# Kernel optimization log

Hardware: AMD Instinct MI355X
Metric: run time of the kernel (lower is better)

## Reference

```python
import jax, jax.numpy as jnp
import numpy as np

B, LE, LD = 8, 4096, 4096
DE, DD, A = 512, 512, 128


def setup_inputs() -> dict:
    key = jax.random.key(0)
    ks = jax.random.split(key, 9)
    f32 = jnp.float32
    return {
        "encoder_outputs": jax.random.normal(ks[0], (B, LE, DE), f32),
        "decoder_outputs": jax.random.normal(ks[1], (B, LD, DD), f32),
        # linear_q / linear_k / linear_v (Dense with bias, relu activation)
        "Wq": jax.random.normal(ks[2], (DD, A), f32) * 0.05,
        "bq": jnp.zeros((A,), f32),
        "Wk": jax.random.normal(ks[3], (DE, A), f32) * 0.05,
        "bk": jnp.zeros((A,), f32),
        "Wv": jax.random.normal(ks[4], (DE, A), f32) * 0.05,
        "bv": jnp.zeros((A,), f32),
        # perceptron branch weights (Dense, no bias)
        "Pw": jax.random.normal(ks[5], (A, A), f32) * 0.05,
        "Pu": jax.random.normal(ks[6], (A, A), f32) * 0.05,
        "pv": jax.random.normal(ks[7], (A, 1), f32) * 0.05,
    }


def reference(encoder_outputs, decoder_outputs, Wq, bq, Wk, bk, Wv, bv, Pw, Pu, pv):
    att = Wq.shape[1]
    q = jax.nn.relu(decoder_outputs @ Wq + bq)   # [B, Ld, A]
    k = jax.nn.relu(encoder_outputs @ Wk + bk)   # [B, Le, A]
    v = jax.nn.relu(encoder_outputs @ Wv + bv)   # [B, Le, A]
    # perceptron score: pv^T (Pw q_i + Pu k_j). No nonlinearity between the
    # sum and pv, so it decomposes additively -> no [B,Ld,Le,A] tiling needed.
    q_term = (q @ Pw) @ pv                        # [B, Ld, 1]
    k_term = (k @ Pu) @ pv                        # [B, Le, 1]
    scores = (q_term + jnp.swapaxes(k_term, 1, 2)) / jnp.sqrt(jnp.float32(att))  # [B, Ld, Le]
    weights = jax.nn.softmax(scores, axis=-1)
    attention = jnp.einsum('bij,bjd->bid', weights, v)  # [B, Ld, A]
    return attention
```

## Files before the change

kernel.cpp:

```cpp
#include <hip/hip_runtime.h>
#include <hip/hip_bf16.h>

#define B_   8
#define LE_  4096
#define LD_  4096
#define KDIM 512
#define AA_  128
#define RTOT (B_*LE_)
#define NDIM 256

typedef __attribute__((ext_vector_type(8))) short short8;
typedef __attribute__((ext_vector_type(4))) float f32x4;

#define WCT_OFF   0
#define U_OFF     262144
#define BIAS_OFF  262656
#define NUM_OFF   263680
#define S_OFF     267776
#define WN_OFF    398848
#define VB_OFF    529920

__device__ inline ushort f2bf(float f) {
    union { float f; unsigned u; } x; x.f = f;
    unsigned r = x.u + 0x7fffu + ((x.u >> 16) & 1u);
    return (ushort)(r >> 16);
}
__device__ inline float bf2f(ushort s) {
    union { unsigned u; float f; } x; x.u = ((unsigned)s) << 16;
    return x.f;
}

__global__ void prep_kernel(const float* __restrict__ Wk, const float* __restrict__ bk,
                            const float* __restrict__ Wv, const float* __restrict__ bv,
                            const float* __restrict__ Pu, const float* __restrict__ pv,
                            ushort* __restrict__ wct, float* __restrict__ u,
                            float* __restrict__ bias, float* __restrict__ num) {
    int t = threadIdx.x;
    int base = blockIdx.x * 256 + t;
    for (int i = 0; i < 4; ++i) {
        int idx = base + i * 32768;
        int n = idx >> 9, k = idx & 511;
        float s = (n < 128) ? Wk[k * 128 + n] : Wv[k * 128 + (n - 128)];
        wct[idx] = f2bf(s);
    }
    if (blockIdx.x == 0) {
        if (t < 128) {
            float acc = 0.f;
            for (int c = 0; c < 128; ++c) acc += Pu[t * 128 + c] * pv[c];
            u[t] = acc;
        }
        bias[t] = (t < 128) ? bk[t] : bv[t - 128];
        for (int i = 0; i < 4; ++i) num[t + i * 256] = 0.f;
    }
}

__global__ __launch_bounds__(512, 4)
void gemm_fused(const float* __restrict__ enc, const ushort* __restrict__ wct,
                const float* __restrict__ bias, const float* __restrict__ u,
                ushort* __restrict__ vbuf, float* __restrict__ sout) {
    __shared__ ushort As[64][72];
    __shared__ ushort Bs[256][72];
    __shared__ float s_red[64][2];
    const int t = threadIdx.x;
    const int wv = t >> 6, l = t & 63;
    const int wm = wv >> 2, wn = wv & 3;
    const int m = l & 15, kb = l >> 4;
    const int row0 = blockIdx.x * 64;

    f32x4 acc[2][4] = {};

    for (int k0 = 0; k0 < KDIM; k0 += 64) {
        {
            int r = t >> 3, k8 = (t & 7) * 8;
            const float4* src = (const float4*)(enc + (size_t)(row0 + r) * KDIM + k0 + k8);
            float4 a0 = src[0], a1 = src[1];
            int4 pk;
            pk.x = (int)f2bf(a0.x) | ((int)f2bf(a0.y) << 16);
            pk.y = (int)f2bf(a0.z) | ((int)f2bf(a0.w) << 16);
            pk.z = (int)f2bf(a1.x) | ((int)f2bf(a1.y) << 16);
            pk.w = (int)f2bf(a1.z) | ((int)f2bf(a1.w) << 16);
            *(int4*)&As[r][k8] = pk;
        }
#pragma unroll
        for (int i = 0; i < 4; ++i) {
            int c = t + i * 512;
            int n = c >> 3, k8 = (c & 7) * 8;
            *(int4*)&Bs[n][k8] = *(const int4*)(wct + (size_t)n * KDIM + k0 + k8);
        }
        __syncthreads();
#pragma unroll
        for (int kc = 0; kc < 2; ++kc) {
            short8 afr[2], bfr[4];
#pragma unroll
            for (int mt = 0; mt < 2; ++mt)
                afr[mt] = *(const short8*)&As[wm * 32 + mt * 16 + m][kc * 32 + kb * 8];
#pragma unroll
            for (int nt = 0; nt < 4; ++nt)
                bfr[nt] = *(const short8*)&Bs[wn * 64 + nt * 16 + m][kc * 32 + kb * 8];
#pragma unroll
            for (int mt = 0; mt < 2; ++mt)
#pragma unroll
                for (int nt = 0; nt < 4; ++nt)
                    acc[mt][nt] = __builtin_amdgcn_mfma_f32_16x16x32_bf16(
                        afr[mt], bfr[nt], acc[mt][nt], 0, 0, 0);
        }
        __syncthreads();
    }

    const int rg = l >> 4;
    if (wn >= 2) {
#pragma unroll
        for (int mt = 0; mt < 2; ++mt) {
#pragma unroll
            for (int nt = 0; nt < 4; ++nt) {
                int col = wn * 64 + nt * 16 + m;
                float bsv = bias[col];
#pragma unroll
                for (int j = 0; j < 4; ++j) {
                    int rowl = wm * 32 + mt * 16 + rg * 4 + j;
                    float v = acc[mt][nt][j] + bsv;
                    v = v > 0.f ? v : 0.f;
                    vbuf[(size_t)(row0 + rowl) * AA_ + (col - 128)] = f2bf(v);
                }
            }
        }
    } else {
#pragma unroll
        for (int mt = 0; mt < 2; ++mt) {
            float p[4] = {0.f, 0.f, 0.f, 0.f};
#pragma unroll
            for (int nt = 0; nt < 4; ++nt) {
                int col = wn * 64 + nt * 16 + m;
                float bsv = bias[col];
                float uw = u[col];
#pragma unroll
                for (int j = 0; j < 4; ++j) {
                    float v = acc[mt][nt][j] + bsv;
                    v = v > 0.f ? v : 0.f;
                    p[j] += v * uw;
                }
            }
#pragma unroll
            for (int j = 0; j < 4; ++j) {
                p[j] += __shfl_xor(p[j], 1);
                p[j] += __shfl_xor(p[j], 2);
                p[j] += __shfl_xor(p[j], 4);
                p[j] += __shfl_xor(p[j], 8);
            }
            if (m == 0) {
#pragma unroll
                for (int j = 0; j < 4; ++j)
                    s_red[wm * 32 + mt * 16 + rg * 4 + j][wn] = p[j];
            }
        }
    }
    __syncthreads();
    if (t < 64) sout[row0 + t] = s_red[t][0] + s_red[t][1];
}

__global__ __launch_bounds__(1024)
void softmax_kernel(const float* __restrict__ s, float* __restrict__ wnorm) {
    __shared__ float red[17];
    int b = blockIdx.x, t = threadIdx.x;
    int l = t & 63, wv = t >> 6;
    const float inv_s = 0.08838834764831843f;
    float v[4], m = -1e30f;
#pragma unroll
    for (int i = 0; i < 4; ++i) {
        v[i] = s[b * 4096 + i * 1024 + t];
        m = fmaxf(m, v[i]);
    }
#pragma unroll
    for (int off = 1; off < 64; off <<= 1) m = fmaxf(m, __shfl_xor(m, off));
    if (l == 0) red[wv] = m;
    __syncthreads();
    if (t == 0) {
        float x = red[0];
        for (int i = 1; i < 16; ++i) x = fmaxf(x, red[i]);
        red[16] = x;
    }
    __syncthreads();
    float M = red[16];
    __syncthreads();
    float e[4], sum = 0.f;
#pragma unroll
    for (int i = 0; i < 4; ++i) {
        e[i] = __expf((v[i] - M) * inv_s);
        sum += e[i];
    }
#pragma unroll
    for (int off = 1; off < 64; off <<= 1) sum += __shfl_xor(sum, off);
    if (l == 0) red[wv] = sum;
    __syncthreads();
    if (t == 0) {
        float x = 0.f;
        for (int i = 0; i < 16; ++i) x += red[i];
        red[16] = 1.0f / x;
    }
    __syncthreads();
    float rS = red[16];
#pragma unroll
    for (int i = 0; i < 4; ++i)
        wnorm[b * 4096 + i * 1024 + t] = e[i] * rS;
}

__global__ __launch_bounds__(256)
void wsum_kernel(const ushort* __restrict__ vbuf, const float* __restrict__ wnorm,
                 float* __restrict__ num) {
    int b = blockIdx.x >> 3, ch = blockIdx.x & 7;
    int t = threadIdx.x, wv = t >> 6, l = t & 63;
    int rg = l >> 4, d8 = (l & 15) * 8;
    int rbase = b * 4096 + ch * 512;
    float acc[8] = {};
    for (int it = 0; it < 32; ++it) {
        int r = rbase + it * 16 + wv * 4 + rg;
        float wj = wnorm[r];
        short8 vv = *(const short8*)(vbuf + (size_t)r * AA_ + d8);
#pragma unroll
        for (int j = 0; j < 8; ++j)
            acc[j] += wj * bf2f((ushort)vv[j]);
    }
#pragma unroll
    for (int j = 0; j < 8; ++j) {
        acc[j] += __shfl_xor(acc[j], 16);
        acc[j] += __shfl_xor(acc[j], 32);
    }
    if (l < 16) {
#pragma unroll
        for (int j = 0; j < 8; ++j)
            atomicAdd(&num[b * AA_ + d8 + j], acc[j]);
    }
}

__global__ void bcast_kernel(const float* __restrict__ num, float4* __restrict__ out) {
    int g = blockIdx.x * 256 + threadIdx.x;
    const float4* n4 = (const float4*)num;
    const int total4 = B_ * LD_ * AA_ / 4;
    for (int c = g; c < total4; c += 524288) {
        int flat = c * 4;
        int b = flat >> 19;
        int d = flat & 127;
        out[c] = n4[b * 32 + (d >> 2)];
    }
}

extern "C" void kernel_launch(void* const* d_in, const int* in_sizes, int n_in,
                              void* d_out, int out_size, void* d_ws, size_t ws_size,
                              hipStream_t stream) {
    const float* enc = (const float*)d_in[0];
    const float* Wk = (const float*)d_in[4];
    const float* bk = (const float*)d_in[5];
    const float* Wv = (const float*)d_in[6];
    const float* bv = (const float*)d_in[7];
    const float* Pu = (const float*)d_in[9];
    const float* pv = (const float*)d_in[10];

    char* ws = (char*)d_ws;
    ushort* wct   = (ushort*)(ws + WCT_OFF);
    float*  u     = (float*)(ws + U_OFF);
    float*  bias  = (float*)(ws + BIAS_OFF);
    float*  num   = (float*)(ws + NUM_OFF);
    float*  s     = (float*)(ws + S_OFF);
    float*  wnorm = (float*)(ws + WN_OFF);
    ushort* vbuf  = (ushort*)(ws + VB_OFF);

    prep_kernel<<<128, 256, 0, stream>>>(Wk, bk, Wv, bv, Pu, pv, wct, u, bias, num);
    gemm_fused<<<RTOT / 64, 512, 0, stream>>>(enc, wct, bias, u, vbuf, s);
    softmax_kernel<<<B_, 1024, 0, stream>>>(s, wnorm);
    wsum_kernel<<<B_ * 8, 256, 0, stream>>>(vbuf, wnorm, num);
    bcast_kernel<<<2048, 256, 0, stream>>>(num, (float4*)d_out);
}
```

Baseline: 184.1 us.

## Fuse GEMM, softmax, weighted sum and broadcast into one cooperative kernel

Replaces the GEMM, softmax, weighted-sum and broadcast kernels with a single cooperative kernel of 256 blocks, each owning 128 rows. The V values stay in registers across grid syncs instead of being written to and reread from a bf16 buffer. Each block recomputes the batch softmax statistics redundantly, and the GEMM loop now register-double-buffers the global loads. This removes several launches and the V round trip through memory, at the cost of two grid-wide barriers and lower occupancy from 128-row tiles with more accumulators.

```diff
diff --git a/kernel.cpp b/kernel.cpp
--- a/kernel.cpp
+++ b/kernel.cpp
@@ -1,13 +1,15 @@
 #include <hip/hip_runtime.h>
 #include <hip/hip_bf16.h>
+#include <hip/hip_cooperative_groups.h>
+
+namespace cg = cooperative_groups;
 
 #define B_   8
-#define LE_  4096
-#define LD_  4096
 #define KDIM 512
 #define AA_  128
-#define RTOT (B_*LE_)
-#define NDIM 256
+#define RTOT 32768
+#define BM   128
+#define NBLK 256
 
 typedef __attribute__((ext_vector_type(8))) short short8;
 typedef __attribute__((ext_vector_type(4))) float f32x4;
@@ -17,17 +19,11 @@
 #define BIAS_OFF  262656
 #define NUM_OFF   263680
 #define S_OFF     267776
-#define WN_OFF    398848
-#define VB_OFF    529920
 
 __device__ inline ushort f2bf(float f) {
     union { float f; unsigned u; } x; x.f = f;
     unsigned r = x.u + 0x7fffu + ((x.u >> 16) & 1u);
     return (ushort)(r >> 16);
-}
-__device__ inline float bf2f(ushort s) {
-    union { unsigned u; float f; } x; x.u = ((unsigned)s) << 16;
-    return x.f;
 }
 
 __global__ void prep_kernel(const float* __restrict__ Wk, const float* __restrict__ bk,
@@ -54,90 +50,117 @@
     }
 }
 
-__global__ __launch_bounds__(512, 4)
-void gemm_fused(const float* __restrict__ enc, const ushort* __restrict__ wct,
-                const float* __restrict__ bias, const float* __restrict__ u,
-                ushort* __restrict__ vbuf, float* __restrict__ sout) {
-    __shared__ ushort As[64][72];
+
+#define LOAD_AB(AV, BV, K0)                                                     \
+    do {                                                                        \
+        _Pragma("unroll")                                                       \
+        for (int i_ = 0; i_ < 2; ++i_) {                                        \
+            int c_ = t + i_ * 512; int r_ = c_ >> 3, k8_ = (c_ & 7) * 8;        \
+            const float4* sp_ = (const float4*)(enc + (size_t)(row0 + r_) * KDIM + (K0) + k8_); \
+            AV[i_][0] = sp_[0]; AV[i_][1] = sp_[1];                             \
+        }                                                                       \
+        _Pragma("unroll")                                                       \
+        for (int i_ = 0; i_ < 4; ++i_) {                                        \
+            int c_ = t + i_ * 512; int n_ = c_ >> 3, k8_ = (c_ & 7) * 8;        \
+            BV[i_] = *(const int4*)(wct + (size_t)n_ * KDIM + (K0) + k8_);      \
+        }                                                                       \
+    } while (0)
+
+#define WRITE_AB(AV, BV)                                                        \
+    do {                                                                        \
+        _Pragma("unroll")                                                       \
+        for (int i_ = 0; i_ < 2; ++i_) {                                        \
+            int c_ = t + i_ * 512; int r_ = c_ >> 3, k8_ = (c_ & 7) * 8;        \
+            int4 pk_;                                                           \
+            pk_.x = (int)f2bf(AV[i_][0].x) | ((int)f2bf(AV[i_][0].y) << 16);    \
+            pk_.y = (int)f2bf(AV[i_][0].z) | ((int)f2bf(AV[i_][0].w) << 16);    \
+            pk_.z = (int)f2bf(AV[i_][1].x) | ((int)f2bf(AV[i_][1].y) << 16);    \
+            pk_.w = (int)f2bf(AV[i_][1].z) | ((int)f2bf(AV[i_][1].w) << 16);    \
+            *(int4*)&As[r_][k8_] = pk_;                                         \
+        }                                                                       \
+        _Pragma("unroll")                                                       \
+        for (int i_ = 0; i_ < 4; ++i_) {                                        \
+            int c_ = t + i_ * 512; int n_ = c_ >> 3, k8_ = (c_ & 7) * 8;        \
+            *(int4*)&Bs[n_][k8_] = BV[i_];                                      \
+        }                                                                       \
+    } while (0)
+
+#define COMPUTE_STEP()                                                          \
+    do {                                                                        \
+        _Pragma("unroll")                                                       \
+        for (int kc_ = 0; kc_ < 2; ++kc_) {                                     \
+            short8 afr_[4], bfr_[4];                                            \
+            _Pragma("unroll")                                                   \
+            for (int mt_ = 0; mt_ < 4; ++mt_)                                   \
+                afr_[mt_] = *(const short8*)&As[wm * 64 + mt_ * 16 + m][kc_ * 32 + kb * 8]; \
+            _Pragma("unroll")                                                   \
+            for (int nt_ = 0; nt_ < 4; ++nt_)                                   \
+                bfr_[nt_] = *(const short8*)&Bs[wn * 64 + nt_ * 16 + m][kc_ * 32 + kb * 8]; \
+            _Pragma("unroll")                                                   \
+            for (int mt_ = 0; mt_ < 4; ++mt_)                                   \
+                _Pragma("unroll")                                               \
+                for (int nt_ = 0; nt_ < 4; ++nt_)                               \
+                    acc[mt_][nt_] = __builtin_amdgcn_mfma_f32_16x16x32_bf16(    \
+                        afr_[mt_], bfr_[nt_], acc[mt_][nt_], 0, 0, 0);          \
+        }                                                                       \
+    } while (0)
+
+__global__ __launch_bounds__(512, 2)
+void mega_kernel(const float* __restrict__ enc, const ushort* __restrict__ wct,
+                 const float* __restrict__ bias, const float* __restrict__ u,
+                 float* __restrict__ sg, float* __restrict__ num,
+                 float* __restrict__ out) {
+    cg::grid_group grid = cg::this_grid();
+    __shared__ ushort As[BM][72];
     __shared__ ushort Bs[256][72];
-    __shared__ float s_red[64][2];
+    __shared__ float sred[256];
+    __shared__ float wl[128];
+    __shared__ float redA[9], redB[9];
+
     const int t = threadIdx.x;
     const int wv = t >> 6, l = t & 63;
     const int wm = wv >> 2, wn = wv & 3;
     const int m = l & 15, kb = l >> 4;
-    const int row0 = blockIdx.x * 64;
-
-    f32x4 acc[2][4] = {};
-
-    for (int k0 = 0; k0 < KDIM; k0 += 64) {
-        {
-            int r = t >> 3, k8 = (t & 7) * 8;
-            const float4* src = (const float4*)(enc + (size_t)(row0 + r) * KDIM + k0 + k8);
-            float4 a0 = src[0], a1 = src[1];
-            int4 pk;
-            pk.x = (int)f2bf(a0.x) | ((int)f2bf(a0.y) << 16);
-            pk.y = (int)f2bf(a0.z) | ((int)f2bf(a0.w) << 16);
-            pk.z = (int)f2bf(a1.x) | ((int)f2bf(a1.y) << 16);
-            pk.w = (int)f2bf(a1.z) | ((int)f2bf(a1.w) << 16);
-            *(int4*)&As[r][k8] = pk;
-        }
-#pragma unroll
-        for (int i = 0; i < 4; ++i) {
-            int c = t + i * 512;
-            int n = c >> 3, k8 = (c & 7) * 8;
-            *(int4*)&Bs[n][k8] = *(const int4*)(wct + (size_t)n * KDIM + k0 + k8);
-        }
-        __syncthreads();
-#pragma unroll
-        for (int kc = 0; kc < 2; ++kc) {
-            short8 afr[2], bfr[4];
-#pragma unroll
-            for (int mt = 0; mt < 2; ++mt)
-                afr[mt] = *(const short8*)&As[wm * 32 + mt * 16 + m][kc * 32 + kb * 8];
-#pragma unroll
-            for (int nt = 0; nt < 4; ++nt)
-                bfr[nt] = *(const short8*)&Bs[wn * 64 + nt * 16 + m][kc * 32 + kb * 8];
-#pragma unroll
-            for (int mt = 0; mt < 2; ++mt)
-#pragma unroll
-                for (int nt = 0; nt < 4; ++nt)
-                    acc[mt][nt] = __builtin_amdgcn_mfma_f32_16x16x32_bf16(
-                        afr[mt], bfr[nt], acc[mt][nt], 0, 0, 0);
-        }
-        __syncthreads();
-    }
-
-    const int rg = l >> 4;
-    if (wn >= 2) {
-#pragma unroll
-        for (int mt = 0; mt < 2; ++mt) {
+    const int rg = kb;
+    const int row0 = blockIdx.x * BM;
+    const int b = row0 >> 12;
+
+    f32x4 acc[4][4] = {};
+
+    {
+        float4 avA[2][2], avB[2][2];
+        int4 bvA[4], bvB[4];
+        LOAD_AB(avA, bvA, 0);
+#pragma unroll
+        for (int st = 0; st < 8; st += 2) {
+            WRITE_AB(avA, bvA);
+            if (st + 1 < 8) LOAD_AB(avB, bvB, (st + 1) * 64);
+            __syncthreads();
+            COMPUTE_STEP();
+            __syncthreads();
+            if (st + 1 < 8) {
+                WRITE_AB(avB, bvB);
+                if (st + 2 < 8) LOAD_AB(avA, bvA, (st + 2) * 64);
+                __syncthreads();
+                COMPUTE_STEP();
+                __syncthreads();
+            }
+        }
+    }
+
+    if (wn < 2) {
+#pragma unroll
+        for (int mt = 0; mt < 4; ++mt) {
+            float p[4] = {0.f, 0.f, 0.f, 0.f};
 #pragma unroll
             for (int nt = 0; nt < 4; ++nt) {
                 int col = wn * 64 + nt * 16 + m;
-                float bsv = bias[col];
+                float bsv = bias[col], uw = u[col];
 #pragma unroll
                 for (int j = 0; j < 4; ++j) {
-                    int rowl = wm * 32 + mt * 16 + rg * 4 + j;
-                    float v = acc[mt][nt][j] + bsv;
-                    v = v > 0.f ? v : 0.f;
-                    vbuf[(size_t)(row0 + rowl) * AA_ + (col - 128)] = f2bf(v);
-                }
-            }
-        }
-    } else {
-#pragma unroll
-        for (int mt = 0; mt < 2; ++mt) {
-            float p[4] = {0.f, 0.f, 0.f, 0.f};
-#pragma unroll
-            for (int nt = 0; nt < 4; ++nt) {
-                int col = wn * 64 + nt * 16 + m;
-                float bsv = bias[col];
-                float uw = u[col];
-#pragma unroll
-                for (int j = 0; j < 4; ++j) {
-                    float v = acc[mt][nt][j] + bsv;
-                    v = v > 0.f ? v : 0.f;
-                    p[j] += v * uw;
+                    float vv = acc[mt][nt][j] + bsv;
+                    vv = vv > 0.f ? vv : 0.f;
+                    p[j] += vv * uw;
                 }
             }
 #pragma unroll
@@ -150,97 +173,90 @@
             if (m == 0) {
 #pragma unroll
                 for (int j = 0; j < 4; ++j)
-                    s_red[wm * 32 + mt * 16 + rg * 4 + j][wn] = p[j];
-            }
-        }
-    }
-    __syncthreads();
-    if (t < 64) sout[row0 + t] = s_red[t][0] + s_red[t][1];
-}
-
-__global__ __launch_bounds__(1024)
-void softmax_kernel(const float* __restrict__ s, float* __restrict__ wnorm) {
-    __shared__ float red[17];
-    int b = blockIdx.x, t = threadIdx.x;
-    int l = t & 63, wv = t >> 6;
+                    sred[(wm * 64 + mt * 16 + rg * 4 + j) * 2 + wn] = p[j];
+            }
+        }
+    } else {
+#pragma unroll
+        for (int mt = 0; mt < 4; ++mt)
+#pragma unroll
+            for (int nt = 0; nt < 4; ++nt) {
+                int col = wn * 64 + nt * 16 + m;
+                float bsv = bias[col];
+#pragma unroll
+                for (int j = 0; j < 4; ++j) {
+                    float vv = acc[mt][nt][j] + bsv;
+                    acc[mt][nt][j] = vv > 0.f ? vv : 0.f;
+                }
+            }
+    }
+    __syncthreads();
+    if (t < 128) sg[row0 + t] = sred[t * 2] + sred[t * 2 + 1];
+
+    grid.sync();
+
     const float inv_s = 0.08838834764831843f;
-    float v[4], m = -1e30f;
-#pragma unroll
-    for (int i = 0; i < 4; ++i) {
-        v[i] = s[b * 4096 + i * 1024 + t];
-        m = fmaxf(m, v[i]);
-    }
-#pragma unroll
-    for (int off = 1; off < 64; off <<= 1) m = fmaxf(m, __shfl_xor(m, off));
-    if (l == 0) red[wv] = m;
+    float vloc[8], mx = -1e30f;
+#pragma unroll
+    for (int it = 0; it < 8; ++it) {
+        vloc[it] = sg[b * 4096 + it * 512 + t];
+        mx = fmaxf(mx, vloc[it]);
+    }
+#pragma unroll
+    for (int off = 1; off < 64; off <<= 1) mx = fmaxf(mx, __shfl_xor(mx, off));
+    if (l == 0) redA[wv] = mx;
     __syncthreads();
     if (t == 0) {
-        float x = red[0];
-        for (int i = 1; i < 16; ++i) x = fmaxf(x, red[i]);
-        red[16] = x;
-    }
-    __syncthreads();
-    float M = red[16];
-    __syncthreads();
-    float e[4], sum = 0.f;
-#pragma unroll
-    for (int i = 0; i < 4; ++i) {
-        e[i] = __expf((v[i] - M) * inv_s);
-        sum += e[i];
-    }
-#pragma unroll
-    for (int off = 1; off < 64; off <<= 1) sum += __shfl_xor(sum, off);
-    if (l == 0) red[wv] = sum;
+        float x = redA[0];
+        for (int i = 1; i < 8; ++i) x = fmaxf(x, redA[i]);
+        redA[8] = x;
+    }
+    __syncthreads();
+    float M = redA[8];
+    float sm = 0.f;
+#pragma unroll
+    for (int it = 0; it < 8; ++it) sm += __expf((vloc[it] - M) * inv_s);
+#pragma unroll
+    for (int off = 1; off < 64; off <<= 1) sm += __shfl_xor(sm, off);
+    if (l == 0) redB[wv] = sm;
     __syncthreads();
     if (t == 0) {
         float x = 0.f;
-        for (int i = 0; i < 16; ++i) x += red[i];
-        red[16] = 1.0f / x;
-    }
-    __syncthreads();
-    float rS = red[16];
-#pragma unroll
-    for (int i = 0; i < 4; ++i)
-        wnorm[b * 4096 + i * 1024 + t] = e[i] * rS;
-}
-
-__global__ __launch_bounds__(256)
-void wsum_kernel(const ushort* __restrict__ vbuf, const float* __restrict__ wnorm,
-                 float* __restrict__ num) {
-    int b = blockIdx.x >> 3, ch = blockIdx.x & 7;
-    int t = threadIdx.x, wv = t >> 6, l = t & 63;
-    int rg = l >> 4, d8 = (l & 15) * 8;
-    int rbase = b * 4096 + ch * 512;
-    float acc[8] = {};
-    for (int it = 0; it < 32; ++it) {
-        int r = rbase + it * 16 + wv * 4 + rg;
-        float wj = wnorm[r];
-        short8 vv = *(const short8*)(vbuf + (size_t)r * AA_ + d8);
-#pragma unroll
-        for (int j = 0; j < 8; ++j)
-            acc[j] += wj * bf2f((ushort)vv[j]);
-    }
-#pragma unroll
-    for (int j = 0; j < 8; ++j) {
-        acc[j] += __shfl_xor(acc[j], 16);
-        acc[j] += __shfl_xor(acc[j], 32);
-    }
-    if (l < 16) {
-#pragma unroll
-        for (int j = 0; j < 8; ++j)
-            atomicAdd(&num[b * AA_ + d8 + j], acc[j]);
-    }
-}
-
-__global__ void bcast_kernel(const float* __restrict__ num, float4* __restrict__ out) {
-    int g = blockIdx.x * 256 + threadIdx.x;
-    const float4* n4 = (const float4*)num;
-    const int total4 = B_ * LD_ * AA_ / 4;
-    for (int c = g; c < total4; c += 524288) {
-        int flat = c * 4;
-        int b = flat >> 19;
-        int d = flat & 127;
-        out[c] = n4[b * 32 + (d >> 2)];
+        for (int i = 0; i < 8; ++i) x += redB[i];
+        redB[8] = 1.0f / x;
+    }
+    __syncthreads();
+    float rS = redB[8];
+    if (t < 128) wl[t] = __expf((sg[row0 + t] - M) * inv_s) * rS;
+    __syncthreads();
+
+    if (wn >= 2) {
+#pragma unroll
+        for (int nt = 0; nt < 4; ++nt) {
+            float p = 0.f;
+#pragma unroll
+            for (int mt = 0; mt < 4; ++mt)
+#pragma unroll
+                for (int j = 0; j < 4; ++j)
+                    p += wl[wm * 64 + mt * 16 + rg * 4 + j] * acc[mt][nt][j];
+            p += __shfl_xor(p, 16);
+            p += __shfl_xor(p, 32);
+            if (l < 16) sred[wm * 128 + (wn - 2) * 64 + nt * 16 + m] = p;
+        }
+    }
+    __syncthreads();
+    if (t < 128) atomicAdd(&num[b * 128 + t], sred[t] + sred[128 + t]);
+
+    grid.sync();
+
+    {
+        const float4* n4 = (const float4*)num;
+        float4* o4 = (float4*)out;
+        float4 nv = n4[b * 32 + (t & 31)];
+        size_t base = (size_t)blockIdx.x * 4096;
+#pragma unroll
+        for (int it = 0; it < 8; ++it)
+            o4[base + it * 512 + t] = nv;
     }
 }
 
@@ -256,17 +272,17 @@
     const float* pv = (const float*)d_in[10];
 
     char* ws = (char*)d_ws;
-    ushort* wct   = (ushort*)(ws + WCT_OFF);
-    float*  u     = (float*)(ws + U_OFF);
-    float*  bias  = (float*)(ws + BIAS_OFF);
-    float*  num   = (float*)(ws + NUM_OFF);
-    float*  s     = (float*)(ws + S_OFF);
-    float*  wnorm = (float*)(ws + WN_OFF);
-    ushort* vbuf  = (ushort*)(ws + VB_OFF);
+    ushort* wct  = (ushort*)(ws + WCT_OFF);
+    float*  u    = (float*)(ws + U_OFF);
+    float*  bias = (float*)(ws + BIAS_OFF);
+    float*  num  = (float*)(ws + NUM_OFF);
+    float*  sg   = (float*)(ws + S_OFF);
+    float*  out  = (float*)d_out;
 
     prep_kernel<<<128, 256, 0, stream>>>(Wk, bk, Wv, bv, Pu, pv, wct, u, bias, num);
-    gemm_fused<<<RTOT / 64, 512, 0, stream>>>(enc, wct, bias, u, vbuf, s);
-    softmax_kernel<<<B_, 1024, 0, stream>>>(s, wnorm);
-    wsum_kernel<<<B_ * 8, 256, 0, stream>>>(vbuf, wnorm, num);
-    bcast_kernel<<<2048, 256, 0, stream>>>(num, (float4*)d_out);
-}
+
+    void* args[7] = {(void*)&enc, (void*)&wct, (void*)&bias, (void*)&u,
+                     (void*)&sg, (void*)&num, (void*)&out};
+    hipLaunchCooperativeKernel((void*)mega_kernel, dim3(NBLK), dim3(512),
+                               args, 0, stream);
+}
```

Result: slower. 263.1 us (+43.0%).

## Fuse softmax into weighted sum, prefetch GEMM tiles into registers, drop atomics

Applied to the files above, without the earlier changes.

Folds the softmax kernel into the weighted-sum kernel: each block recomputes the per-batch max and sum over the 4096 scores and builds weights on the fly. This removes one launch and the wnorm buffer. The per-block partial sums go to a parts buffer instead of atomics, so the num zeroing in prep goes away, and the broadcast kernel reduces the 8 partials per block. The GEMM now register-prefetches the next K-slice of encoder and weights before its MFMAs to overlap global loads with compute, at the cost of higher register pressure and redundant softmax reductions.

```diff
diff --git a/kernel.cpp b/kernel.cpp
--- a/kernel.cpp
+++ b/kernel.cpp
@@ -2,11 +2,9 @@
 #include <hip/hip_bf16.h>
 
 #define B_   8
-#define LE_  4096
-#define LD_  4096
 #define KDIM 512
 #define AA_  128
-#define RTOT (B_*LE_)
+#define RTOT 32768
 #define NDIM 256
 
 typedef __attribute__((ext_vector_type(8))) short short8;
@@ -15,10 +13,9 @@
 #define WCT_OFF   0
 #define U_OFF     262144
 #define BIAS_OFF  262656
-#define NUM_OFF   263680
-#define S_OFF     267776
-#define WN_OFF    398848
-#define VB_OFF    529920
+#define PARTS_OFF 263680
+#define S_OFF     296448
+#define VB_OFF    427520
 
 __device__ inline ushort f2bf(float f) {
     union { float f; unsigned u; } x; x.f = f;
@@ -34,7 +31,7 @@
                             const float* __restrict__ Wv, const float* __restrict__ bv,
                             const float* __restrict__ Pu, const float* __restrict__ pv,
                             ushort* __restrict__ wct, float* __restrict__ u,
-                            float* __restrict__ bias, float* __restrict__ num) {
+                            float* __restrict__ bias) {
     int t = threadIdx.x;
     int base = blockIdx.x * 256 + t;
     for (int i = 0; i < 4; ++i) {
@@ -50,7 +47,6 @@
             u[t] = acc;
         }
         bias[t] = (t < 128) ? bk[t] : bv[t - 128];
-        for (int i = 0; i < 4; ++i) num[t + i * 256] = 0.f;
     }
 }
 
@@ -67,27 +63,46 @@
     const int m = l & 15, kb = l >> 4;
     const int row0 = blockIdx.x * 64;
 
+    const int ar = t >> 3, ak8 = (t & 7) * 8;
+    const float* aptr = enc + (size_t)(row0 + ar) * KDIM + ak8;
+
     f32x4 acc[2][4] = {};
-
-    for (int k0 = 0; k0 < KDIM; k0 += 64) {
+    float4 a0, a1;
+    int4 bp[4];
+
+    a0 = *(const float4*)aptr;
+    a1 = *(const float4*)(aptr + 4);
+#pragma unroll
+    for (int i = 0; i < 4; ++i) {
+        int c = t + i * 512, n = c >> 3, k8 = (c & 7) * 8;
+        bp[i] = *(const int4*)(wct + (size_t)n * KDIM + k8);
+    }
+
+    for (int st = 0; st < 8; ++st) {
         {
-            int r = t >> 3, k8 = (t & 7) * 8;
-            const float4* src = (const float4*)(enc + (size_t)(row0 + r) * KDIM + k0 + k8);
-            float4 a0 = src[0], a1 = src[1];
             int4 pk;
             pk.x = (int)f2bf(a0.x) | ((int)f2bf(a0.y) << 16);
             pk.y = (int)f2bf(a0.z) | ((int)f2bf(a0.w) << 16);
             pk.z = (int)f2bf(a1.x) | ((int)f2bf(a1.y) << 16);
             pk.w = (int)f2bf(a1.z) | ((int)f2bf(a1.w) << 16);
-            *(int4*)&As[r][k8] = pk;
-        }
-#pragma unroll
-        for (int i = 0; i < 4; ++i) {
-            int c = t + i * 512;
-            int n = c >> 3, k8 = (c & 7) * 8;
-            *(int4*)&Bs[n][k8] = *(const int4*)(wct + (size_t)n * KDIM + k0 + k8);
+            *(int4*)&As[ar][ak8] = pk;
+#pragma unroll
+            for (int i = 0; i < 4; ++i) {
+                int c = t + i * 512, n = c >> 3, k8 = (c & 7) * 8;
+                *(int4*)&Bs[n][k8] = bp[i];
+            }
         }
         __syncthreads();
+        if (st < 7) {
+            const float* ap = aptr + (st + 1) * 64;
+            a0 = *(const float4*)ap;
+            a1 = *(const float4*)(ap + 4);
+#pragma unroll
+            for (int i = 0; i < 4; ++i) {
+                int c = t + i * 512, n = c >> 3, k8 = (c & 7) * 8;
+                bp[i] = *(const int4*)(wct + (size_t)n * KDIM + (st + 1) * 64 + k8);
+            }
+        }
 #pragma unroll
         for (int kc = 0; kc < 2; ++kc) {
             short8 afr[2], bfr[4];
@@ -107,37 +122,20 @@
         __syncthreads();
     }
 
-    const int rg = l >> 4;
-    if (wn >= 2) {
+    const int rg = kb;
+    if (wn < 2) {
 #pragma unroll
         for (int mt = 0; mt < 2; ++mt) {
+            float p[4] = {0.f, 0.f, 0.f, 0.f};
 #pragma unroll
             for (int nt = 0; nt < 4; ++nt) {
                 int col = wn * 64 + nt * 16 + m;
-                float bsv = bias[col];
+                float bsv = bias[col], uw = u[col];
 #pragma unroll
                 for (int j = 0; j < 4; ++j) {
-                    int rowl = wm * 32 + mt * 16 + rg * 4 + j;
-                    float v = acc[mt][nt][j] + bsv;
-                    v = v > 0.f ? v : 0.f;
-                    vbuf[(size_t)(row0 + rowl) * AA_ + (col - 128)] = f2bf(v);
-                }
-            }
-        }
-    } else {
-#pragma unroll
-        for (int mt = 0; mt < 2; ++mt) {
-            float p[4] = {0.f, 0.f, 0.f, 0.f};
-#pragma unroll
-            for (int nt = 0; nt < 4; ++nt) {
-                int col = wn * 64 + nt * 16 + m;
-                float bsv = bias[col];
-                float uw = u[col];
-#pragma unroll
-                for (int j = 0; j < 4; ++j) {
-                    float v = acc[mt][nt][j] + bsv;
-                    v = v > 0.f ? v : 0.f;
-                    p[j] += v * uw;
+                    float vvv = acc[mt][nt][j] + bsv;
+                    vvv = vvv > 0.f ? vvv : 0.f;
+                    p[j] += vvv * uw;
                 }
             }
 #pragma unroll
@@ -153,72 +151,71 @@
                     s_red[wm * 32 + mt * 16 + rg * 4 + j][wn] = p[j];
             }
         }
+    } else {
+#pragma unroll
+        for (int mt = 0; mt < 2; ++mt) {
+#pragma unroll
+            for (int nt = 0; nt < 4; ++nt) {
+                int col = wn * 64 + nt * 16 + m;
+                float bsv = bias[col];
+#pragma unroll
+                for (int j = 0; j < 4; ++j) {
+                    int rowl = wm * 32 + mt * 16 + rg * 4 + j;
+                    float vvv = acc[mt][nt][j] + bsv;
+                    vvv = vvv > 0.f ? vvv : 0.f;
+                    vbuf[(size_t)(row0 + rowl) * AA_ + (col - 128)] = f2bf(vvv);
+                }
+            }
+        }
     }
     __syncthreads();
     if (t < 64) sout[row0 + t] = s_red[t][0] + s_red[t][1];
 }
 
-__global__ __launch_bounds__(1024)
-void softmax_kernel(const float* __restrict__ s, float* __restrict__ wnorm) {
-    __shared__ float red[17];
-    int b = blockIdx.x, t = threadIdx.x;
-    int l = t & 63, wv = t >> 6;
+__global__ __launch_bounds__(256)
+void wsum_kernel(const ushort* __restrict__ vbuf, const float* __restrict__ sg,
+                 float* __restrict__ parts) {
+    __shared__ float redM[5], redS[5];
+    __shared__ float pw[4][128];
+    const int blk = blockIdx.x;
+    const int b = blk >> 3, ch = blk & 7;
+    const int t = threadIdx.x, wv = t >> 6, l = t & 63;
     const float inv_s = 0.08838834764831843f;
-    float v[4], m = -1e30f;
-#pragma unroll
-    for (int i = 0; i < 4; ++i) {
-        v[i] = s[b * 4096 + i * 1024 + t];
-        m = fmaxf(m, v[i]);
-    }
-#pragma unroll
-    for (int off = 1; off < 64; off <<= 1) m = fmaxf(m, __shfl_xor(m, off));
-    if (l == 0) red[wv] = m;
-    __syncthreads();
-    if (t == 0) {
-        float x = red[0];
-        for (int i = 1; i < 16; ++i) x = fmaxf(x, red[i]);
-        red[16] = x;
-    }
-    __syncthreads();
-    float M = red[16];
-    __syncthreads();
-    float e[4], sum = 0.f;
-#pragma unroll
-    for (int i = 0; i < 4; ++i) {
-        e[i] = __expf((v[i] - M) * inv_s);
-        sum += e[i];
-    }
-#pragma unroll
-    for (int off = 1; off < 64; off <<= 1) sum += __shfl_xor(sum, off);
-    if (l == 0) red[wv] = sum;
-    __syncthreads();
-    if (t == 0) {
-        float x = 0.f;
-        for (int i = 0; i < 16; ++i) x += red[i];
-        red[16] = 1.0f / x;
-    }
-    __syncthreads();
-    float rS = red[16];
-#pragma unroll
-    for (int i = 0; i < 4; ++i)
-        wnorm[b * 4096 + i * 1024 + t] = e[i] * rS;
-}
-
-__global__ __launch_bounds__(256)
-void wsum_kernel(const ushort* __restrict__ vbuf, const float* __restrict__ wnorm,
-                 float* __restrict__ num) {
-    int b = blockIdx.x >> 3, ch = blockIdx.x & 7;
-    int t = threadIdx.x, wv = t >> 6, l = t & 63;
-    int rg = l >> 4, d8 = (l & 15) * 8;
-    int rbase = b * 4096 + ch * 512;
+
+    float vl[16], mx = -1e30f;
+#pragma unroll
+    for (int i = 0; i < 16; ++i) {
+        vl[i] = sg[b * 4096 + i * 256 + t];
+        mx = fmaxf(mx, vl[i]);
+    }
+#pragma unroll
+    for (int off = 1; off < 64; off <<= 1) mx = fmaxf(mx, __shfl_xor(mx, off));
+    if (l == 0) redM[wv] = mx;
+    __syncthreads();
+    if (t == 0) redM[4] = fmaxf(fmaxf(redM[0], redM[1]), fmaxf(redM[2], redM[3]));
+    __syncthreads();
+    const float M = redM[4];
+    float sm = 0.f;
+#pragma unroll
+    for (int i = 0; i < 16; ++i) sm += __expf((vl[i] - M) * inv_s);
+#pragma unroll
+    for (int off = 1; off < 64; off <<= 1) sm += __shfl_xor(sm, off);
+    if (l == 0) redS[wv] = sm;
+    __syncthreads();
+    if (t == 0) redS[4] = 1.0f / (redS[0] + redS[1] + redS[2] + redS[3]);
+    __syncthreads();
+    const float rS = redS[4];
+
+    const int rg = l >> 4, d8 = (l & 15) * 8;
+    const int rbase = b * 4096 + ch * 512;
     float acc[8] = {};
     for (int it = 0; it < 32; ++it) {
         int r = rbase + it * 16 + wv * 4 + rg;
-        float wj = wnorm[r];
-        short8 vv = *(const short8*)(vbuf + (size_t)r * AA_ + d8);
+        float wj = __expf((sg[r] - M) * inv_s) * rS;
+        short8 vvv = *(const short8*)(vbuf + (size_t)r * AA_ + d8);
 #pragma unroll
         for (int j = 0; j < 8; ++j)
-            acc[j] += wj * bf2f((ushort)vv[j]);
+            acc[j] += wj * bf2f((ushort)vvv[j]);
     }
 #pragma unroll
     for (int j = 0; j < 8; ++j) {
@@ -227,21 +224,30 @@
     }
     if (l < 16) {
 #pragma unroll
-        for (int j = 0; j < 8; ++j)
-            atomicAdd(&num[b * AA_ + d8 + j], acc[j]);
-    }
-}
-
-__global__ void bcast_kernel(const float* __restrict__ num, float4* __restrict__ out) {
-    int g = blockIdx.x * 256 + threadIdx.x;
-    const float4* n4 = (const float4*)num;
-    const int total4 = B_ * LD_ * AA_ / 4;
-    for (int c = g; c < total4; c += 524288) {
-        int flat = c * 4;
-        int b = flat >> 19;
-        int d = flat & 127;
-        out[c] = n4[b * 32 + (d >> 2)];
-    }
+        for (int j = 0; j < 8; ++j) pw[wv][d8 + j] = acc[j];
+    }
+    __syncthreads();
+    if (t < 128) parts[blk * 128 + t] = pw[0][t] + pw[1][t] + pw[2][t] + pw[3][t];
+}
+
+__global__ __launch_bounds__(256)
+void bcast_kernel(const float* __restrict__ parts, float4* __restrict__ out) {
+    __shared__ float4 nv[32];
+    const int t = threadIdx.x;
+    const int c = blockIdx.x * 256 + t;
+    const int b = (blockIdx.x * 1024) >> 19;
+    if (t < 32) {
+        const float4* p4 = (const float4*)parts;
+        float4 s = {0.f, 0.f, 0.f, 0.f};
+#pragma unroll
+        for (int ch = 0; ch < 8; ++ch) {
+            float4 q = p4[(b * 8 + ch) * 32 + t];
+            s.x += q.x; s.y += q.y; s.z += q.z; s.w += q.w;
+        }
+        nv[t] = s;
+    }
+    __syncthreads();
+    out[c] = nv[t & 31];
 }
 
 extern "C" void kernel_launch(void* const* d_in, const int* in_sizes, int n_in,
@@ -259,14 +265,12 @@
     ushort* wct   = (ushort*)(ws + WCT_OFF);
     float*  u     = (float*)(ws + U_OFF);
     float*  bias  = (float*)(ws + BIAS_OFF);
-    float*  num   = (float*)(ws + NUM_OFF);
-    float*  s     = (float*)(ws + S_OFF);
-    float*  wnorm = (float*)(ws + WN_OFF);
+    float*  parts = (float*)(ws + PARTS_OFF);
+    float*  sg    = (float*)(ws + S_OFF);
     ushort* vbuf  = (ushort*)(ws + VB_OFF);
 
-    prep_kernel<<<128, 256, 0, stream>>>(Wk, bk, Wv, bv, Pu, pv, wct, u, bias, num);
-    gemm_fused<<<RTOT / 64, 512, 0, stream>>>(enc, wct, bias, u, vbuf, s);
-    softmax_kernel<<<B_, 1024, 0, stream>>>(s, wnorm);
-    wsum_kernel<<<B_ * 8, 256, 0, stream>>>(vbuf, wnorm, num);
-    bcast_kernel<<<2048, 256, 0, stream>>>(num, (float4*)d_out);
-}
+    prep_kernel<<<128, 256, 0, stream>>>(Wk, bk, Wv, bv, Pu, pv, wct, u, bias);
+    gemm_fused<<<RTOT / 64, 512, 0, stream>>>(enc, wct, bias, u, vbuf, sg);
+    wsum_kernel<<<64, 256, 0, stream>>>(vbuf, sg, parts);
+    bcast_kernel<<<4096, 256, 0, stream>>>(parts, (float4*)d_out);
+}
```

New measurement: 214.3 us. 16.4% more time.
